# Optimization experiments

Hardware: AMD Instinct MI355X
Metric: run time of the kernel (lower is better)

The kernel has to match this reference:

```python
import jax, jax.numpy as jnp
import numpy as np

B, T, N, D = 16, 1024, 1024, 256   # batch, query len (hp.max_T), key len (hp.max_N), hp.d
WIN = 64                            # hp.attention_win_size
NEG = jnp.float32(-2**32 + 1)       # padding value used by the TF module


def setup_inputs() -> dict:
    key = jax.random.key(0)
    k1, k2, k3, k4 = jax.random.split(key, 4)
    Q = jax.random.normal(k1, (B, T, D), dtype=jnp.float32)
    K = jax.random.normal(k2, (B, N, D), dtype=jnp.float32)
    V = jax.random.normal(k3, (B, N, D), dtype=jnp.float32)
    prev_max_attentions = jax.random.randint(k4, (B,), 0, N - WIN, dtype=jnp.int64)
    return {"Q": Q, "K": K, "V": V, "prev_max_attentions": prev_max_attentions}


def reference(Q, K, V, prev_max_attentions):
    # scaled scores: [B, T, N]
    A = jnp.einsum("btd,bnd->btn", Q, K) * jax.lax.rsqrt(jnp.float32(D))

    # monotonic window mask (mono_attention=True):
    idx = jnp.arange(N)                              # [N]
    prev = prev_max_attentions[:, None]              # [B, 1]
    masks = (idx < prev) | (idx >= prev + WIN)       # [B, N], True = disallowed
    A = jnp.where(masks[:, None, :], NEG, A)         # broadcast over T (== tf.tile)

    A = jax.nn.softmax(A, axis=-1)                   # [B, T, N]
    max_attentions = jnp.argmax(A, axis=-1).astype(jnp.float32)  # [B, T]

    R = jnp.concatenate([jnp.einsum("btn,bnd->btd", A, V), Q], axis=-1)  # [B, T, 2D]
    alignments = jnp.transpose(A, (0, 2, 1))         # [B, N, T]
    return (R, alignments, max_attentions)
```

## Files before the change

kernel.cpp:

```cpp
#include <hip/hip_runtime.h>


#define BB 16
#define TT 1024
#define NN 1024
#define DD 256
#define WIN 64
#define TBLK 16
#define NT 256
#define NZ 240

#define R_ELEMS   (16u*1024u*512u)
#define ALN_ELEMS (16u*1024u*1024u)

#define LSTR 132

typedef float f32x4 __attribute__((ext_vector_type(4)));

__device__ __forceinline__ void nts4(void* p, float4 v) {
    f32x4 nv;
    nv.x = v.x; nv.y = v.y; nv.z = v.z; nv.w = v.w;
    __builtin_nontemporal_store(nv, (f32x4*)p);
}

__global__ __launch_bounds__(NT, 4) void attn_v14(
    const float* __restrict__ Q, const float* __restrict__ K,
    const float* __restrict__ V, const int* __restrict__ prev_in,
    float* __restrict__ out)
{
    __shared__ float ks[WIN * LSTR];
    __shared__ float p_lds[TBLK][WIN + 4];

    float* Rout   = out;
    float* aligns = out + R_ELEMS;
    float* maxatt = out + R_ELEMS + ALN_ELEMS;

    const int tid = threadIdx.x;

    if (blockIdx.x < NZ) {
        const int zb    = blockIdx.x;
        const int b     = zb / 15;
        const int chunk = zb % 15;
        const int prev  = prev_in[b];
        float* zbase = aligns + (size_t)b * NN * TT;
        const float4 z = make_float4(0.f, 0.f, 0.f, 0.f);
        #pragma unroll 8
        for (int r = 0; r < 64; ++r) {
            int idx = chunk * 64 + r;
            int n   = idx < prev ? idx : idx + WIN;
            nts4(zbase + (size_t)n * 1024 + tid * 4, z);
        }
        return;
    }

    const int aid  = blockIdx.x - NZ;
    const int lane = tid & 63;
    const int w    = __builtin_amdgcn_readfirstlane(tid >> 6);
    const int b    = aid >> 6;
    const int t0   = (aid & 63) * TBLK;
    const int prev = prev_in[b];

    const float* qb = Q + ((size_t)b * TT + t0 + 4 * w) * DD;

    #pragma unroll
    for (int t = 0; t < 4; ++t) {
        float4 qv = ((const float4*)(qb + t * DD))[lane];
        float* Rrow = Rout + ((size_t)b * TT + t0 + 4 * w + t) * (2 * DD);
        nts4(Rrow + DD + lane * 4, qv);
    }

    float acc[4] = {0.f, 0.f, 0.f, 0.f};
    #pragma unroll
    for (int h = 0; h < 2; ++h) {
        if (h) __syncthreads();
        const float4* Ksrc = (const float4*)(K + ((size_t)b * NN + prev) * DD + h * 128);
        #pragma unroll
        for (int k = 0; k < 8; ++k) {
            int t4 = tid + k * NT;
            int r = t4 >> 5, c = t4 & 31;
            float4 v = Ksrc[(size_t)r * 64 + c];
            *(float4*)&ks[r * LSTR + c * 4] = v;
        }
        __syncthreads();

        const float* qh = qb + h * 128;
        #pragma unroll 8
        for (int d4 = 0; d4 < 32; ++d4) {
            float4 kk = *(const float4*)&ks[lane * LSTR + d4 * 4];
            #pragma unroll
            for (int t = 0; t < 4; ++t) {
                float4 q = ((const float4*)(qh + t * DD))[d4];
                acc[t] = fmaf(q.x, kk.x, fmaf(q.y, kk.y, fmaf(q.z, kk.z, fmaf(q.w, kk.w, acc[t]))));
            }
        }
    }

    #pragma unroll
    for (int t = 0; t < 4; ++t) {
        float v = acc[t] * 0.0625f;

        float m = v;
        #pragma unroll
        for (int off = 32; off; off >>= 1) m = fmaxf(m, __shfl_xor(m, off));

        float e = expf(v - m);
        float s = e;
        #pragma unroll
        for (int off = 32; off; off >>= 1) s += __shfl_xor(s, off);

        p_lds[4 * w + t][lane] = e / s;

        float av = v; int ai = lane;
        #pragma unroll
        for (int off = 32; off; off >>= 1) {
            float ov = __shfl_xor(av, off);
            int   oi = __shfl_xor(ai, off);
            if (ov > av || (ov == av && oi < ai)) { av = ov; ai = oi; }
        }
        if (lane == 0)
            __builtin_nontemporal_store((float)(prev + ai),
                                        &maxatt[(size_t)b * TT + t0 + 4 * w + t]);
    }
    __syncthreads();

    {
        const int j = tid >> 2, cg = tid & 3;
        float4 v;
        v.x = p_lds[cg * 4 + 0][j];
        v.y = p_lds[cg * 4 + 1][j];
        v.z = p_lds[cg * 4 + 2][j];
        v.w = p_lds[cg * 4 + 3][j];
        nts4(aligns + ((size_t)b * NN + prev + j) * TT + t0 + cg * 4, v);
    }

    {
        const float4* V4 = (const float4*)(V + ((size_t)b * NN + prev) * DD);
        float4 o[4];
        #pragma unroll
        for (int t = 0; t < 4; ++t) o[t] = make_float4(0.f, 0.f, 0.f, 0.f);

        #pragma unroll 4
        for (int j4 = 0; j4 < WIN / 4; ++j4) {
            float4 p0 = *(const float4*)&p_lds[4 * w + 0][j4 * 4];
            float4 p1 = *(const float4*)&p_lds[4 * w + 1][j4 * 4];
            float4 p2 = *(const float4*)&p_lds[4 * w + 2][j4 * 4];
            float4 p3 = *(const float4*)&p_lds[4 * w + 3][j4 * 4];
            float4 v0 = V4[(size_t)(j4 * 4 + 0) * 64 + lane];
            float4 v1 = V4[(size_t)(j4 * 4 + 1) * 64 + lane];
            float4 v2 = V4[(size_t)(j4 * 4 + 2) * 64 + lane];
            float4 v3 = V4[(size_t)(j4 * 4 + 3) * 64 + lane];
            #define ACC4(o_, p_) \
                o_.x = fmaf(p_.x, v0.x, fmaf(p_.y, v1.x, fmaf(p_.z, v2.x, fmaf(p_.w, v3.x, o_.x)))); \
                o_.y = fmaf(p_.x, v0.y, fmaf(p_.y, v1.y, fmaf(p_.z, v2.y, fmaf(p_.w, v3.y, o_.y)))); \
                o_.z = fmaf(p_.x, v0.z, fmaf(p_.y, v1.z, fmaf(p_.z, v2.z, fmaf(p_.w, v3.z, o_.z)))); \
                o_.w = fmaf(p_.x, v0.w, fmaf(p_.y, v1.w, fmaf(p_.z, v2.w, fmaf(p_.w, v3.w, o_.w))));
            ACC4(o[0], p0) ACC4(o[1], p1) ACC4(o[2], p2) ACC4(o[3], p3)
            #undef ACC4
        }

        #pragma unroll
        for (int t = 0; t < 4; ++t) {
            float* Rrow = Rout + ((size_t)b * TT + t0 + 4 * w + t) * (2 * DD);
            nts4(Rrow + lane * 4, o[t]);
        }
    }
}

extern "C" void kernel_launch(void* const* d_in, const int* in_sizes, int n_in,
                              void* d_out, int out_size, void* d_ws, size_t ws_size,
                              hipStream_t stream) {
    const float* Q = (const float*)d_in[0];
    const float* K = (const float*)d_in[1];
    const float* V = (const float*)d_in[2];
    const int* prev = (const int*)d_in[3];
    float* out = (float*)d_out;

    attn_v14<<<NZ + BB * TT / TBLK, NT, 0, stream>>>(Q, K, V, prev, out);
}
```

Baseline: 158.7 us.

## Split PV product across waves by D-slice and key groups with shuffle reduction

The P·V stage is restructured. Before, each wave handled 4 query rows and read all 64 V rows across the full D width. Now each wave owns a 64-wide D slice for all 16 query rows, and its lanes split the 64 keys into 4 groups of 16. Partial sums are combined with cross-lane shuffles. Each V element is loaded once per block instead of once per wave, at the cost of 64 accumulator registers, 64 extra shuffles and a predicated store pattern.

```diff
diff --git a/kernel.cpp b/kernel.cpp
--- a/kernel.cpp
+++ b/kernel.cpp
@@ -23,7 +23,7 @@
     __builtin_nontemporal_store(nv, (f32x4*)p);
 }
 
-__global__ __launch_bounds__(NT, 4) void attn_v14(
+__global__ __launch_bounds__(NT, 4) void attn_v17(
     const float* __restrict__ Q, const float* __restrict__ K,
     const float* __restrict__ V, const int* __restrict__ prev_in,
     float* __restrict__ out)
@@ -134,34 +134,44 @@
     }
 
     {
-        const float4* V4 = (const float4*)(V + ((size_t)b * NN + prev) * DD);
-        float4 o[4];
+        const int jj = lane >> 4;
+        const int d4 = lane & 15;
+        const float* Vq = V + ((size_t)b * NN + prev + jj * 16) * DD + w * 64 + d4 * 4;
+
+        float4 o[16];
         #pragma unroll
-        for (int t = 0; t < 4; ++t) o[t] = make_float4(0.f, 0.f, 0.f, 0.f);
+        for (int t = 0; t < 16; ++t) o[t] = make_float4(0.f, 0.f, 0.f, 0.f);
 
-        #pragma unroll 4
-        for (int j4 = 0; j4 < WIN / 4; ++j4) {
-            float4 p0 = *(const float4*)&p_lds[4 * w + 0][j4 * 4];
-            float4 p1 = *(const float4*)&p_lds[4 * w + 1][j4 * 4];
-            float4 p2 = *(const float4*)&p_lds[4 * w + 2][j4 * 4];
-            float4 p3 = *(const float4*)&p_lds[4 * w + 3][j4 * 4];
-            float4 v0 = V4[(size_t)(j4 * 4 + 0) * 64 + lane];
-            float4 v1 = V4[(size_t)(j4 * 4 + 1) * 64 + lane];
-            float4 v2 = V4[(size_t)(j4 * 4 + 2) * 64 + lane];
-            float4 v3 = V4[(size_t)(j4 * 4 + 3) * 64 + lane];
-            #define ACC4(o_, p_) \
-                o_.x = fmaf(p_.x, v0.x, fmaf(p_.y, v1.x, fmaf(p_.z, v2.x, fmaf(p_.w, v3.x, o_.x)))); \
-                o_.y = fmaf(p_.x, v0.y, fmaf(p_.y, v1.y, fmaf(p_.z, v2.y, fmaf(p_.w, v3.y, o_.y)))); \
-                o_.z = fmaf(p_.x, v0.z, fmaf(p_.y, v1.z, fmaf(p_.z, v2.z, fmaf(p_.w, v3.z, o_.z)))); \
-                o_.w = fmaf(p_.x, v0.w, fmaf(p_.y, v1.w, fmaf(p_.z, v2.w, fmaf(p_.w, v3.w, o_.w))));
-            ACC4(o[0], p0) ACC4(o[1], p1) ACC4(o[2], p2) ACC4(o[3], p3)
-            #undef ACC4
+        #pragma unroll
+        for (int k4 = 0; k4 < 4; ++k4) {
+            float4 vv0 = *(const float4*)(Vq + (size_t)(k4 * 4 + 0) * DD);
+            float4 vv1 = *(const float4*)(Vq + (size_t)(k4 * 4 + 1) * DD);
+            float4 vv2 = *(const float4*)(Vq + (size_t)(k4 * 4 + 2) * DD);
+            float4 vv3 = *(const float4*)(Vq + (size_t)(k4 * 4 + 3) * DD);
+            #pragma unroll
+            for (int t = 0; t < 16; ++t) {
+                float4 p4 = *(const float4*)&p_lds[t][jj * 16 + k4 * 4];
+                o[t].x = fmaf(p4.x, vv0.x, fmaf(p4.y, vv1.x, fmaf(p4.z, vv2.x, fmaf(p4.w, vv3.x, o[t].x))));
+                o[t].y = fmaf(p4.x, vv0.y, fmaf(p4.y, vv1.y, fmaf(p4.z, vv2.y, fmaf(p4.w, vv3.y, o[t].y))));
+                o[t].z = fmaf(p4.x, vv0.z, fmaf(p4.y, vv1.z, fmaf(p4.z, vv2.z, fmaf(p4.w, vv3.z, o[t].z))));
+                o[t].w = fmaf(p4.x, vv0.w, fmaf(p4.y, vv1.w, fmaf(p4.z, vv2.w, fmaf(p4.w, vv3.w, o[t].w))));
+            }
         }
 
         #pragma unroll
-        for (int t = 0; t < 4; ++t) {
-            float* Rrow = Rout + ((size_t)b * TT + t0 + 4 * w + t) * (2 * DD);
-            nts4(Rrow + lane * 4, o[t]);
+        for (int t = 0; t < 16; ++t) {
+            o[t].x += __shfl_xor(o[t].x, 16); o[t].x += __shfl_xor(o[t].x, 32);
+            o[t].y += __shfl_xor(o[t].y, 16); o[t].y += __shfl_xor(o[t].y, 32);
+            o[t].z += __shfl_xor(o[t].z, 16); o[t].z += __shfl_xor(o[t].z, 32);
+            o[t].w += __shfl_xor(o[t].w, 16); o[t].w += __shfl_xor(o[t].w, 32);
+        }
+
+        #pragma unroll
+        for (int t = 0; t < 16; ++t) {
+            if (jj == (t >> 2)) {
+                float* Rp = Rout + ((size_t)b * TT + t0 + t) * (2 * DD) + w * 64 + d4 * 4;
+                nts4(Rp, o[t]);
+            }
         }
     }
 }
@@ -175,5 +185,5 @@
     const int* prev = (const int*)d_in[3];
     float* out = (float*)d_out;
 
-    attn_v14<<<NZ + BB * TT / TBLK, NT, 0, stream>>>(Q, K, V, prev, out);
+    attn_v17<<<NZ + BB * TT / TBLK, NT, 0, stream>>>(Q, K, V, prev, out);
 }
```

New measurement: 193.2 us. 21.7% more time.
